# Optimization experiments

Measured on AMD Instinct MI355X. Metric: run time of the kernel, lower is better.

## Reference

```python
import jax, jax.numpy as jnp
import numpy as np

T, D, N, K, H = 2048, 4096, 32, 8, 128
ROPE_THETA = 500000.0


def setup_inputs() -> dict:
    key = jax.random.key(0)
    ks = jax.random.split(key, 5)
    s = 0.02
    return {
        "x": jax.random.normal(ks[0], (T, D), jnp.float32) * s,
        "positions": jnp.arange(T, dtype=jnp.int64 if jax.config.jax_enable_x64 else jnp.int32),
        "Wq": jax.random.normal(ks[1], (D, N, H), jnp.float32) * s,
        "Wk": jax.random.normal(ks[2], (D, K, H), jnp.float32) * s,
        "Wv": jax.random.normal(ks[3], (D, K, H), jnp.float32) * s,
        "Wo": jax.random.normal(ks[4], (N, H, D), jnp.float32) * s,
    }


def _rope(positions, q, k):
    # positions: [T]; q: [T,N,H]; k: [T,K,H]. Half-split rotation (Llama style).
    half = H // 2
    inv_freq = 1.0 / (ROPE_THETA ** (jnp.arange(0, half, dtype=jnp.float32) / half))
    ang = positions.astype(jnp.float32)[:, None] * inv_freq  # [T, H/2]
    cos = jnp.cos(ang)[:, None, :]  # [T,1,H/2]
    sin = jnp.sin(ang)[:, None, :]

    def rot(x):
        x1, x2 = x[..., :half], x[..., half:]
        return jnp.concatenate([x1 * cos - x2 * sin, x2 * cos + x1 * sin], axis=-1)

    return rot(q), rot(k)


def reference(x, positions, Wq, Wk, Wv, Wo):
    q = jnp.einsum('td,dnh->tnh', x, Wq)  # [T,N,H]
    k = jnp.einsum('td,dkh->tkh', x, Wk)  # [T,K,H]
    v = jnp.einsum('td,dkh->tkh', x, Wv)
    q, k = _rope(positions, q, k)

    rep = N // K  # GQA: expand kv heads to query heads
    kr = jnp.repeat(k, rep, axis=1)  # [T,N,H]
    vr = jnp.repeat(v, rep, axis=1)

    scale = 1.0 / jnp.sqrt(jnp.asarray(H, jnp.float32))
    scores = jnp.einsum('tnh,snh->nts', q, kr) * scale  # [N,T,T]
    causal = positions[:, None] >= positions[None, :]   # [T,T]
    scores = jnp.where(causal[None, :, :], scores, jnp.finfo(scores.dtype).min)
    probs = jax.nn.softmax(scores, axis=-1)
    ctx = jnp.einsum('nts,snh->tnh', probs, vr)  # [T,N,H]
    return jnp.einsum('tnh,nhd->td', ctx, Wo)
```

## Files before the change

kernel.cpp:

```cpp
#include <hip/hip_runtime.h>
#include <hip/hip_bf16.h>

#define T_SEQ 2048
#define D_MODEL 4096
#define N_HEADS 32
#define K_HEADS 8
#define HEAD_DIM 128

typedef unsigned short u16;
typedef short sfrag8 __attribute__((ext_vector_type(8)));
typedef float ffrag4 __attribute__((ext_vector_type(4)));

#if defined(__has_builtin)
#  if __has_builtin(__builtin_amdgcn_exp2f)
#    define EXP2F(x) __builtin_amdgcn_exp2f(x)
#  else
#    define EXP2F(x) exp2f(x)
#  endif
#else
#  define EXP2F(x) exp2f(x)
#endif

#define QSCALE_LOG2E 0.12751744900463627f
#define NEG_L2_THETA_64 (-0.29580575889569f)

__device__ __forceinline__ float bf2f(u16 u) {
    return __uint_as_float(((unsigned int)u) << 16);
}
__device__ __forceinline__ u16 f2bf(float f) {
    unsigned int x = __float_as_uint(f);
    unsigned int r = (x + 0x7fffu + ((x >> 16) & 1u)) >> 16;
    return (u16)r;
}
__device__ __forceinline__ uint4 pack8(const float4 a, const float4 b) {
    uint4 r;
    r.x = (unsigned)f2bf(a.x) | ((unsigned)f2bf(a.y) << 16);
    r.y = (unsigned)f2bf(a.z) | ((unsigned)f2bf(a.w) << 16);
    r.z = (unsigned)f2bf(b.x) | ((unsigned)f2bf(b.y) << 16);
    r.w = (unsigned)f2bf(b.z) | ((unsigned)f2bf(b.w) << 16);
    return r;
}

__device__ __forceinline__ void gload_lds16(const u16* g, u16* l) {
    __builtin_amdgcn_global_load_lds(
        (const __attribute__((address_space(1))) void*)g,
        (__attribute__((address_space(3))) void*)l, 16, 0, 0);
}

__global__ __launch_bounds__(256) void convert_bf16(
    const float* __restrict__ X, u16* __restrict__ Y, int n8)
{
    const int i = blockIdx.x * 256 + threadIdx.x;
    if (i < n8) {
        float4 a = ((const float4*)X)[(size_t)i * 2];
        float4 b = ((const float4*)X)[(size_t)i * 2 + 1];
        ((uint4*)Y)[i] = pack8(a, b);
    }
}

__global__ __launch_bounds__(256) void transpose_f32_bf16(
    const float* __restrict__ W, u16* __restrict__ WT, int R, int C)
{
    __shared__ float Ts[64][65];
    const int t = threadIdx.x;
    const int c0 = blockIdx.x * 64, r0 = blockIdx.y * 64;
    const int rl = t >> 4, cl = (t & 15) * 4;
#pragma unroll
    for (int p = 0; p < 4; ++p) {
        const int r = p * 16 + rl;
        float4 v = *(const float4*)(W + (size_t)(r0 + r) * C + c0 + cl);
        Ts[r][cl] = v.x; Ts[r][cl + 1] = v.y; Ts[r][cl + 2] = v.z; Ts[r][cl + 3] = v.w;
    }
    __syncthreads();
    const int nl = t >> 2, k4 = (t & 3) * 16;
    u16 tmp[16];
#pragma unroll
    for (int j = 0; j < 16; ++j) tmp[j] = f2bf(Ts[k4 + j][nl]);
    u16* dst = WT + (size_t)(c0 + nl) * R + r0 + k4;
    *(uint4*)(dst) = *(uint4*)&tmp[0];
    *(uint4*)(dst + 8) = *(uint4*)&tmp[8];
}

template <int CMODE>
__global__ __launch_bounds__(256) void gemm_bt(
    const u16* __restrict__ A, const u16* __restrict__ BT,
    void* __restrict__ Cp, int M, int Nb, int Kd, int ldc)
{
    __shared__ __align__(16) u16 SmemAll[2 * 128 * 64];
    u16* As = SmemAll;
    u16* Bs = SmemAll + 128 * 64;

    const int tid = threadIdx.x;
    const int lane = tid & 63;
    const int w = tid >> 6;
    const int wm = w >> 1, wn = w & 1;
    const int ln = lane & 15, quad = lane >> 4;

    int wid = blockIdx.y * gridDim.x + blockIdx.x;
    const int nwg = gridDim.x * gridDim.y;
    const int cpx = nwg >> 3;
    wid = (wid & 7) * cpx + (wid >> 3);
    const int bx = wid % gridDim.x;
    const int by = wid / gridDim.x;

    const int m0 = by * 128, n0 = bx * 128;

    size_t aoff[4], boff[4];
#pragma unroll
    for (int i = 0; i < 4; ++i) {
        const int row = (i * 4 + w) * 8 + (lane >> 3);
        const int cg = (lane & 7) ^ (lane >> 3);
        aoff[i] = (size_t)(m0 + row) * Kd + cg * 8;
        boff[i] = (size_t)(n0 + row) * Kd + cg * 8;
    }

    ffrag4 acc[4][4];
#pragma unroll
    for (int mi = 0; mi < 4; ++mi)
#pragma unroll
        for (int ni = 0; ni < 4; ++ni) acc[mi][ni] = (ffrag4){0.f, 0.f, 0.f, 0.f};

    for (int k0 = 0; k0 < Kd; k0 += 64) {
#pragma unroll
        for (int i = 0; i < 4; ++i) {
            gload_lds16(A + aoff[i] + k0, &As[(i * 4 + w) * 512]);
            gload_lds16(BT + boff[i] + k0, &Bs[(i * 4 + w) * 512]);
        }
        __syncthreads();

#pragma unroll
        for (int kk = 0; kk < 2; ++kk) {
            sfrag8 af[4], bfv[4];
#pragma unroll
            for (int mi = 0; mi < 4; ++mi) {
                const int row = wm * 64 + mi * 16 + ln;
                const int pc = ((kk * 4) | quad) ^ (ln & 7);
                af[mi] = *(const sfrag8*)&As[row * 64 + pc * 8];
            }
#pragma unroll
            for (int ni = 0; ni < 4; ++ni) {
                const int row = wn * 64 + ni * 16 + ln;
                const int pc = ((kk * 4) | quad) ^ (ln & 7);
                bfv[ni] = *(const sfrag8*)&Bs[row * 64 + pc * 8];
            }
#pragma unroll
            for (int mi = 0; mi < 4; ++mi)
#pragma unroll
                for (int ni = 0; ni < 4; ++ni)
                    acc[mi][ni] = __builtin_amdgcn_mfma_f32_16x16x32_bf16(
                        af[mi], bfv[ni], acc[mi][ni], 0, 0, 0);
        }
        __syncthreads();
    }

    if constexpr (CMODE == 4) {
        u16* base = (u16*)Cp;
        if (n0 < 5120) {
#pragma unroll
            for (int mi = 0; mi < 4; ++mi)
#pragma unroll
                for (int ni = 0; ni < 4; ++ni) {
                    const int colL = wn * 64 + ni * 16 + ln;
#pragma unroll
                    for (int i = 0; i < 4; ++i) {
                        const int rowL = wm * 64 + mi * 16 + quad * 4 + i;
                        SmemAll[rowL * 128 + colL] = f2bf(acc[mi][ni][i]);
                    }
                }
            __syncthreads();
            float invf[4];
#pragma unroll
            for (int ni = 0; ni < 4; ++ni)
                invf[ni] = EXP2F((float)(ni * 16 + ln) * NEG_L2_THETA_64);
#pragma unroll
            for (int mi = 0; mi < 4; ++mi)
#pragma unroll
                for (int ni = 0; ni < 4; ++ni) {
                    const int colL = wn * 64 + ni * 16 + ln;
                    const int fi = colL & 63;
                    const int gcol = n0 + colL;
#pragma unroll
                    for (int i = 0; i < 4; ++i) {
                        const int rowL = wm * 64 + mi * 16 + quad * 4 + i;
                        const int grow = m0 + rowL;
                        const float x1 = bf2f(SmemAll[rowL * 128 + fi]);
                        const float x2 = bf2f(SmemAll[rowL * 128 + fi + 64]);
                        const float ang = (float)grow * invf[ni];
                        const float cw = cosf(ang);
                        const float sw = sinf(ang);
                        const float o = (wn == 0) ? (x1 * cw - x2 * sw)
                                                  : (x2 * cw + x1 * sw);
                        const u16 v = f2bf(o);
                        if (gcol < 4096) {
                            base[4194304u + (size_t)grow * 4096 + gcol] = v;
                        } else {
                            base[(size_t)grow * 1024 + (gcol - 4096)] = v;
                        }
                    }
                }
        } else {
#pragma unroll
            for (int mi = 0; mi < 4; ++mi)
#pragma unroll
                for (int ni = 0; ni < 4; ++ni) {
                    const int gcol = n0 + wn * 64 + ni * 16 + ln;
#pragma unroll
                    for (int i = 0; i < 4; ++i) {
                        const int grow = m0 + wm * 64 + mi * 16 + quad * 4 + i;
                        base[2097152u + (size_t)(gcol - 5120) * T_SEQ + grow] =
                            f2bf(acc[mi][ni][i]);
                    }
                }
        }
        return;
    }

#pragma unroll
    for (int mi = 0; mi < 4; ++mi) {
#pragma unroll
        for (int ni = 0; ni < 4; ++ni) {
            const int gcol = n0 + wn * 64 + ni * 16 + ln;
#pragma unroll
            for (int i = 0; i < 4; ++i) {
                const int grow = m0 + wm * 64 + mi * 16 + quad * 4 + i;
                if constexpr (CMODE == 1) {
                    ((float*)Cp)[(size_t)grow * ldc + gcol] = acc[mi][ni][i];
                } else {
                    ((u16*)Cp)[(size_t)grow * ldc + gcol] = f2bf(acc[mi][ni][i]);
                }
            }
        }
    }
}

template <int AMODE, int CMODE>
__global__ __launch_bounds__(256) void gemm_any(
    const void* __restrict__ Ap, const float* __restrict__ B, void* __restrict__ Cp,
    int M, int Nb, int Kd, int ldc)
{
    __shared__ __align__(16) u16 As[64 * 64];
    __shared__ __align__(16) u16 Bs[64 * 72];

    const int tid = threadIdx.x;
    const int n0 = blockIdx.x * 64, m0 = blockIdx.y * 64;

    const int lr = tid >> 3;
    const int cc8 = tid & 7;
    const int sw = ((cc8 ^ (lr & 7)) * 8);
    const int dstA0 = lr * 64 + sw;
    const int dstA1 = (lr + 32) * 64 + sw;
    const size_t arow0 = (size_t)(m0 + lr) * Kd;
    const size_t arow1 = (size_t)(m0 + lr + 32) * Kd;

    const int kr = tid >> 2;
    const int ncb = (tid & 3) * 16;

    const int lane = tid & 63;
    const int w = tid >> 6;
    const int col16 = lane & 15;
    const int quad = lane >> 4;
    const int swl = lane & 7;
    const int mrow = w * 16 + col16;

    ffrag4 acc[4];
#pragma unroll
    for (int j = 0; j < 4; ++j) acc[j] = (ffrag4){0.f, 0.f, 0.f, 0.f};

    for (int k0 = 0; k0 < Kd; k0 += 64) {
        if constexpr (AMODE == 1) {
            const u16* Af = (const u16*)Ap;
            uint4 va0 = *(const uint4*)(Af + arow0 + k0 + cc8 * 8);
            uint4 va1 = *(const uint4*)(Af + arow1 + k0 + cc8 * 8);
            *(uint4*)&As[dstA0] = va0;
            *(uint4*)&As[dstA1] = va1;
        } else {
            const float* Af = (const float*)Ap;
            float4 a00 = *(const float4*)(Af + arow0 + k0 + cc8 * 8);
            float4 a01 = *(const float4*)(Af + arow0 + k0 + cc8 * 8 + 4);
            float4 a10 = *(const float4*)(Af + arow1 + k0 + cc8 * 8);
            float4 a11 = *(const float4*)(Af + arow1 + k0 + cc8 * 8 + 4);
            *(uint4*)&As[dstA0] = pack8(a00, a01);
            *(uint4*)&As[dstA1] = pack8(a10, a11);
        }
        {
            const float* bp = B + (size_t)(k0 + kr) * Nb + n0 + ncb;
            float4 b0 = *(const float4*)(bp);
            float4 b1 = *(const float4*)(bp + 4);
            float4 b2 = *(const float4*)(bp + 8);
            float4 b3 = *(const float4*)(bp + 12);
            u16 tmp[16];
            tmp[0] = f2bf(b0.x); tmp[1] = f2bf(b0.y); tmp[2] = f2bf(b0.z); tmp[3] = f2bf(b0.w);
            tmp[4] = f2bf(b1.x); tmp[5] = f2bf(b1.y); tmp[6] = f2bf(b1.z); tmp[7] = f2bf(b1.w);
            tmp[8] = f2bf(b2.x); tmp[9] = f2bf(b2.y); tmp[10] = f2bf(b2.z); tmp[11] = f2bf(b2.w);
            tmp[12] = f2bf(b3.x); tmp[13] = f2bf(b3.y); tmp[14] = f2bf(b3.z); tmp[15] = f2bf(b3.w);
#pragma unroll
            for (int e = 0; e < 16; ++e)
                Bs[(ncb + e) * 72 + kr] = tmp[e];
        }
        __syncthreads();
#pragma unroll
        for (int c = 0; c < 2; ++c) {
            const int cc = c * 4 + quad;
            const int koffA = (cc ^ swl) * 8;
            sfrag8 af = *(const sfrag8*)&As[mrow * 64 + koffA];
#pragma unroll
            for (int j = 0; j < 4; ++j) {
                sfrag8 bfv = *(const sfrag8*)&Bs[(j * 16 + col16) * 72 + cc * 8];
                acc[j] = __builtin_amdgcn_mfma_f32_16x16x32_bf16(af, bfv, acc[j], 0, 0, 0);
            }
        }
        __syncthreads();
    }

#pragma unroll
    for (int j = 0; j < 4; ++j) {
        const int gcol = n0 + j * 16 + col16;
#pragma unroll
        for (int i = 0; i < 4; ++i) {
            const int grow = m0 + w * 16 + quad * 4 + i;
            if constexpr (CMODE == 1) {
                ((float*)Cp)[(size_t)grow * ldc + gcol] = acc[j][i];
            } else if constexpr (CMODE == 2) {
                ((u16*)Cp)[(size_t)gcol * ldc + grow] = f2bf(acc[j][i]);
            } else {
                ((u16*)Cp)[(size_t)grow * ldc + gcol] = f2bf(acc[j][i]);
            }
        }
    }
}

__global__ __launch_bounds__(64) void rope_kernel(
    u16* __restrict__ buf, int nheads, int t0)
{
    const int h = blockIdx.x;
    const int t = blockIdx.y;
    u16* rowp = buf + ((size_t)t * nheads + h) * HEAD_DIM;
    const int i = threadIdx.x;
    const float p = (float)(t0 + t);
    const float inv = expf(-((float)i * (1.0f / 64.0f)) * 13.122363377404329f);
    const float ang = p * inv;
    const float c = cosf(ang);
    const float s = sinf(ang);
    const float x1 = bf2f(rowp[i]);
    const float x2 = bf2f(rowp[i + 64]);
    rowp[i] = f2bf(x1 * c - x2 * s);
    rowp[i + 64] = f2bf(x2 * c + x1 * s);
}

__global__ __launch_bounds__(256) void attn_mfma(
    const u16* q, const u16* __restrict__ k,
    const u16* __restrict__ vt, u16* ctx, int t0)
{
    __shared__ __align__(16) u16 Ktb[2][64 * 128];
    __shared__ __align__(16) u16 Vtb[2][128 * 64];
    __shared__ __align__(16) u16 Ps[4][16 * 72];

    const int head = blockIdx.x;
    const int qt = gridDim.y - 1 - blockIdx.y;
    const int kvh = head >> 2;
    const int tid = threadIdx.x;
    const int lane = tid & 63;
    const int w = tid >> 6;
    const int ln = lane & 15;
    const int quad = lane >> 4;

    const int qrow_loc = qt * 64 + w * 16 + ln;
    sfrag8 qf[4];
    {
        const u16* qg = q + ((size_t)qrow_loc * N_HEADS + head) * HEAD_DIM;
#pragma unroll
        for (int kk = 0; kk < 4; ++kk)
            qf[kk] = *(const sfrag8*)(qg + kk * 32 + quad * 8);
    }

    const int krow_l = lane >> 4;
    const int kcl    = lane & 15;
    const int vrow_l = lane >> 3;
    const int vcl    = lane & 7;

    auto stage = [&](int kv0s, int buf) {
#pragma unroll
        for (int i = 0; i < 4; ++i) {
            const int seg = i * 4 + w;
            const int krow = seg * 4 + krow_l;
            const int kcg = kcl ^ (krow & 7);
            gload_lds16(
                k + ((size_t)(kv0s + krow) * K_HEADS + kvh) * HEAD_DIM + kcg * 8,
                &Ktb[buf][seg * 512]);
            const int vrow = seg * 8 + vrow_l;
            const int vcg = vcl ^ (vrow & 7);
            gload_lds16(
                vt + ((size_t)(kvh * 128 + vrow)) * T_SEQ + kv0s + vcg * 8,
                &Vtb[buf][seg * 512]);
        }
    };

    ffrag4 acc_o[8];
#pragma unroll
    for (int dt = 0; dt < 8; ++dt) acc_o[dt] = (ffrag4){0.f, 0.f, 0.f, 0.f};
    float mrow[4] = {-INFINITY, -INFINITY, -INFINITY, -INFINITY};
    float lrow_l[4] = {0.f, 0.f, 0.f, 0.f};

    const int Tq0 = t0 + qt * 64;
    const int nst = Tq0 / 64 + 1;
    const int qabs_base = Tq0 + w * 16 + quad * 4;

    stage(0, 0);
    int cur = 0;

    for (int st = 0; st < nst; ++st) {
        const int kv0 = st * 64;
        const bool diag = (st == nst - 1);

        __syncthreads();
        if (st + 1 < nst) stage(kv0 + 64, cur ^ 1);

        const int ktc = diag ? ((w < 2) ? 2 : 4) : 4;
        ffrag4 sacc[4];
        __builtin_amdgcn_s_setprio(1);
#pragma unroll
        for (int kt = 0; kt < 4; ++kt) {
            if (kt >= ktc) break;
            sacc[kt] = (ffrag4){0.f, 0.f, 0.f, 0.f};
#pragma unroll
            for (int kk = 0; kk < 4; ++kk) {
                sfrag8 bfr = *(const sfrag8*)&Ktb[cur][
                    (kt * 16 + ln) * 128 + (((kk * 4 + quad) ^ (ln & 7)) * 8)];
                sacc[kt] = __builtin_amdgcn_mfma_f32_16x16x32_bf16(qf[kk], bfr, sacc[kt], 0, 0, 0);
            }
        }
        __builtin_amdgcn_s_setprio(0);
        float sv[4][4];
#pragma unroll
        for (int kt = 0; kt < 4; ++kt) {
            if (kt >= ktc) break;
            const int key_abs = kv0 + kt * 16 + ln;
#pragma unroll
            for (int i = 0; i < 4; ++i) {
                float s = sacc[kt][i] * QSCALE_LOG2E;
                if (diag && key_abs > qabs_base + i) s = -INFINITY;
                sv[kt][i] = s;
            }
        }
        bool grew = false;
#pragma unroll
        for (int kt = 0; kt < 4; ++kt) {
            if (kt >= ktc) break;
#pragma unroll
            for (int i = 0; i < 4; ++i)
                grew |= (sv[kt][i] > mrow[i] + 8.0f);
        }
        if (__any(grew)) {
            float tm[4];
#pragma unroll
            for (int i = 0; i < 4; ++i) {
                float t = sv[0][i];
                for (int kt = 1; kt < ktc; ++kt) t = fmaxf(t, sv[kt][i]);
                t = fmaxf(t, __shfl_xor(t, 1));
                t = fmaxf(t, __shfl_xor(t, 2));
                t = fmaxf(t, __shfl_xor(t, 4));
                t = fmaxf(t, __shfl_xor(t, 8));
                tm[i] = t;
            }
            float alpha[4];
#pragma unroll
            for (int i = 0; i < 4; ++i) {
                const float mn = fmaxf(mrow[i], tm[i]);
                alpha[i] = EXP2F(mrow[i] - mn);
                mrow[i] = mn;
            }
            const bool noop = (alpha[0] == 1.f) && (alpha[1] == 1.f) &&
                              (alpha[2] == 1.f) && (alpha[3] == 1.f);
            if (!__all(noop)) {
#pragma unroll
                for (int i = 0; i < 4; ++i) {
                    lrow_l[i] *= alpha[i];
#pragma unroll
                    for (int dt = 0; dt < 8; ++dt) acc_o[dt][i] *= alpha[i];
                }
            }
        }
#pragma unroll
        for (int kt = 0; kt < 4; ++kt) {
            if (kt >= ktc) break;
#pragma unroll
            for (int i = 0; i < 4; ++i) {
                const float p = EXP2F(sv[kt][i] - mrow[i]);
                lrow_l[i] += p;
                Ps[w][(quad * 4 + i) * 72 + kt * 16 + ln] = f2bf(p);
            }
        }
        const int kbm = ktc >> 1;
        __builtin_amdgcn_s_setprio(1);
#pragma unroll
        for (int kb = 0; kb < 2; ++kb) {
            if (kb >= kbm) break;
            sfrag8 afr = *(const sfrag8*)&Ps[w][ln * 72 + kb * 32 + quad * 8];
#pragma unroll
            for (int dt = 0; dt < 8; ++dt) {
                sfrag8 bfr = *(const sfrag8*)&Vtb[cur][
                    (dt * 16 + ln) * 64 + (((kb * 4 + quad) ^ (ln & 7)) * 8)];
                acc_o[dt] = __builtin_amdgcn_mfma_f32_16x16x32_bf16(afr, bfr, acc_o[dt], 0, 0, 0);
            }
        }
        __builtin_amdgcn_s_setprio(0);
        cur ^= 1;
    }

    float invl[4];
#pragma unroll
    for (int i = 0; i < 4; ++i) {
        float t = lrow_l[i];
        t += __shfl_xor(t, 1);
        t += __shfl_xor(t, 2);
        t += __shfl_xor(t, 4);
        t += __shfl_xor(t, 8);
        invl[i] = 1.0f / t;
    }
#pragma unroll
    for (int i = 0; i < 4; ++i) {
        u16* og = ctx + ((size_t)(qt * 64 + w * 16 + quad * 4 + i) * N_HEADS + head) * HEAD_DIM;
#pragma unroll
        for (int dt = 0; dt < 8; ++dt)
            og[dt * 16 + ln] = f2bf(acc_o[dt][i] * invl[i]);
    }
}

extern "C" void kernel_launch(void* const* d_in, const int* in_sizes, int n_in,
                              void* d_out, int out_size, void* d_ws, size_t ws_size,
                              hipStream_t stream) {
    (void)in_sizes; (void)n_in; (void)out_size;
    const float* x  = (const float*)d_in[0];
    const float* Wq = (const float*)d_in[2];
    const float* Wk = (const float*)d_in[3];
    const float* Wv = (const float*)d_in[4];
    const float* Wo = (const float*)d_in[5];
    float* out = (float*)d_out;
    char* ws = (char*)d_ws;
    const size_t MiB = 1024 * 1024;

    if (ws_size >= 88 * MiB) {
        u16* kbuf  = (u16*)(ws);
        u16* vtbuf = (u16*)(ws + 4 * MiB);
        u16* qsl   = (u16*)(ws + 8 * MiB);
        u16* xb    = (u16*)(ws + 24 * MiB);
        u16* WqkvT = (u16*)(ws + 40 * MiB);

        convert_bf16<<<dim3(T_SEQ * D_MODEL / 8 / 256), 256, 0, stream>>>(
            x, xb, T_SEQ * D_MODEL / 8);
        transpose_f32_bf16<<<dim3(64, 64), 256, 0, stream>>>(
            Wq, WqkvT, D_MODEL, N_HEADS * HEAD_DIM);
        transpose_f32_bf16<<<dim3(16, 64), 256, 0, stream>>>(
            Wk, WqkvT + (size_t)4096 * 4096, D_MODEL, K_HEADS * HEAD_DIM);
        transpose_f32_bf16<<<dim3(16, 64), 256, 0, stream>>>(
            Wv, WqkvT + (size_t)5120 * 4096, D_MODEL, K_HEADS * HEAD_DIM);

        gemm_bt<4><<<dim3(48, 16), 256, 0, stream>>>(
            xb, WqkvT, ws, T_SEQ, 6144, D_MODEL, 0);

        attn_mfma<<<dim3(N_HEADS, T_SEQ / 64), 256, 0, stream>>>(
            qsl, kbuf, vtbuf, qsl, 0);

        transpose_f32_bf16<<<dim3(64, 64), 256, 0, stream>>>(
            Wo, WqkvT, N_HEADS * HEAD_DIM, D_MODEL);
        gemm_bt<1><<<dim3(32, 16), 256, 0, stream>>>(
            qsl, WqkvT, out, T_SEQ, D_MODEL, N_HEADS * HEAD_DIM, D_MODEL);
        return;
    }

    u16* kbuf  = (u16*)(ws);
    u16* vtbuf = (u16*)(ws + 4194304);
    u16* qsl   = (u16*)(ws + 8388608);

    int S = 8;
    if (ws_size >= (size_t)8388608 + 16777216)      S = 1;
    else if (ws_size >= (size_t)8388608 + 8388608)  S = 2;
    else if (ws_size >= (size_t)8388608 + 4194304)  S = 4;
    const int Ts = T_SEQ / S;

    gemm_any<0, 0><<<dim3(16, T_SEQ / 64), 256, 0, stream>>>(
        x, Wk, kbuf, T_SEQ, K_HEADS * HEAD_DIM, D_MODEL, K_HEADS * HEAD_DIM);
    gemm_any<0, 2><<<dim3(16, T_SEQ / 64), 256, 0, stream>>>(
        x, Wv, vtbuf, T_SEQ, K_HEADS * HEAD_DIM, D_MODEL, T_SEQ);
    rope_kernel<<<dim3(K_HEADS, T_SEQ), 64, 0, stream>>>(kbuf, K_HEADS, 0);

    for (int s = 0; s < S; ++s) {
        const int t0 = s * Ts;
        gemm_any<0, 0><<<dim3(64, Ts / 64), 256, 0, stream>>>(
            x + (size_t)t0 * D_MODEL, Wq, qsl, Ts, D_MODEL, D_MODEL, D_MODEL);
        rope_kernel<<<dim3(N_HEADS, Ts), 64, 0, stream>>>(qsl, N_HEADS, t0);
        attn_mfma<<<dim3(N_HEADS, Ts / 64), 256, 0, stream>>>(
            qsl, kbuf, vtbuf, qsl, t0);
        gemm_any<1, 1><<<dim3(64, Ts / 64), 256, 0, stream>>>(
            qsl, Wo, out + (size_t)t0 * D_MODEL, Ts, D_MODEL, N_HEADS * HEAD_DIM, D_MODEL);
    }
}
```

Before: 508.9 us.

## Use 128-row query tiles in attention and fuse weight preparation kernels

```diff
diff --git a/kernel.cpp b/kernel.cpp
--- a/kernel.cpp
+++ b/kernel.cpp
@@ -77,6 +77,48 @@
 #pragma unroll
     for (int j = 0; j < 16; ++j) tmp[j] = f2bf(Ts[k4 + j][nl]);
     u16* dst = WT + (size_t)(c0 + nl) * R + r0 + k4;
+    *(uint4*)(dst) = *(uint4*)&tmp[0];
+    *(uint4*)(dst + 8) = *(uint4*)&tmp[8];
+}
+
+__global__ __launch_bounds__(256) void prep_all(
+    const float* __restrict__ x, const float* __restrict__ Wq,
+    const float* __restrict__ Wk, const float* __restrict__ Wv,
+    const float* __restrict__ Wo, u16* __restrict__ xb,
+    u16* __restrict__ WqkvT, u16* __restrict__ WoT)
+{
+    __shared__ float Ts[64][65];
+    const int t = threadIdx.x;
+    int bid = blockIdx.x;
+
+    if (bid < 4096) {
+        const int i = bid * 256 + t;
+        float4 a = ((const float4*)x)[(size_t)i * 2];
+        float4 b = ((const float4*)x)[(size_t)i * 2 + 1];
+        ((uint4*)xb)[i] = pack8(a, b);
+        return;
+    }
+    bid -= 4096;
+    const float* W; u16* WT; int C, bx, by;
+    if (bid < 4096)      { W = Wq; WT = WqkvT;                         C = 4096; bx = bid & 63;          by = bid >> 6; }
+    else if (bid < 5120) { W = Wk; WT = WqkvT + (size_t)4096 * 4096;   C = 1024; bx = (bid - 4096) & 15; by = (bid - 4096) >> 4; }
+    else if (bid < 6144) { W = Wv; WT = WqkvT + (size_t)5120 * 4096;   C = 1024; bx = (bid - 5120) & 15; by = (bid - 5120) >> 4; }
+    else                 { W = Wo; WT = WoT;                           C = 4096; bx = (bid - 6144) & 63; by = (bid - 6144) >> 6; }
+
+    const int c0 = bx * 64, r0 = by * 64;
+    const int rl = t >> 4, cl = (t & 15) * 4;
+#pragma unroll
+    for (int p = 0; p < 4; ++p) {
+        const int r = p * 16 + rl;
+        float4 v = *(const float4*)(W + (size_t)(r0 + r) * C + c0 + cl);
+        Ts[r][cl] = v.x; Ts[r][cl + 1] = v.y; Ts[r][cl + 2] = v.z; Ts[r][cl + 3] = v.w;
+    }
+    __syncthreads();
+    const int nl = t >> 2, k4 = (t & 3) * 16;
+    u16 tmp[16];
+#pragma unroll
+    for (int j = 0; j < 16; ++j) tmp[j] = f2bf(Ts[k4 + j][nl]);
+    u16* dst = WT + (size_t)(c0 + nl) * 4096 + r0 + k4;
     *(uint4*)(dst) = *(uint4*)&tmp[0];
     *(uint4*)(dst + 8) = *(uint4*)&tmp[8];
 }
@@ -347,13 +389,13 @@
     rowp[i + 64] = f2bf(x2 * c + x1 * s);
 }
 
-__global__ __launch_bounds__(256) void attn_mfma(
+__global__ __launch_bounds__(512) void attn_mfma(
     const u16* q, const u16* __restrict__ k,
     const u16* __restrict__ vt, u16* ctx, int t0)
 {
     __shared__ __align__(16) u16 Ktb[2][64 * 128];
     __shared__ __align__(16) u16 Vtb[2][128 * 64];
-    __shared__ __align__(16) u16 Ps[4][16 * 72];
+    __shared__ __align__(16) u16 Ps[8][16 * 72];
 
     const int head = blockIdx.x;
     const int qt = gridDim.y - 1 - blockIdx.y;
@@ -364,7 +406,7 @@
     const int ln = lane & 15;
     const int quad = lane >> 4;
 
-    const int qrow_loc = qt * 64 + w * 16 + ln;
+    const int qrow_loc = qt * 128 + w * 16 + ln;
     sfrag8 qf[4];
     {
         const u16* qg = q + ((size_t)qrow_loc * N_HEADS + head) * HEAD_DIM;
@@ -380,8 +422,8 @@
 
     auto stage = [&](int kv0s, int buf) {
 #pragma unroll
-        for (int i = 0; i < 4; ++i) {
-            const int seg = i * 4 + w;
+        for (int i = 0; i < 2; ++i) {
+            const int seg = i * 8 + w;
             const int krow = seg * 4 + krow_l;
             const int kcg = kcl ^ (krow & 7);
             gload_lds16(
@@ -401,109 +443,113 @@
     float mrow[4] = {-INFINITY, -INFINITY, -INFINITY, -INFINITY};
     float lrow_l[4] = {0.f, 0.f, 0.f, 0.f};
 
-    const int Tq0 = t0 + qt * 64;
-    const int nst = Tq0 / 64 + 1;
+    const int Tq0 = t0 + qt * 128;
+    const int nst = Tq0 / 64 + 2;
     const int qabs_base = Tq0 + w * 16 + quad * 4;
+    const int qlast = Tq0 + w * 16 + 15;
 
     stage(0, 0);
     int cur = 0;
 
     for (int st = 0; st < nst; ++st) {
         const int kv0 = st * 64;
-        const bool diag = (st == nst - 1);
 
         __syncthreads();
         if (st + 1 < nst) stage(kv0 + 64, cur ^ 1);
 
-        const int ktc = diag ? ((w < 2) ? 2 : 4) : 4;
-        ffrag4 sacc[4];
-        __builtin_amdgcn_s_setprio(1);
-#pragma unroll
-        for (int kt = 0; kt < 4; ++kt) {
-            if (kt >= ktc) break;
-            sacc[kt] = (ffrag4){0.f, 0.f, 0.f, 0.f};
-#pragma unroll
-            for (int kk = 0; kk < 4; ++kk) {
-                sfrag8 bfr = *(const sfrag8*)&Ktb[cur][
-                    (kt * 16 + ln) * 128 + (((kk * 4 + quad) ^ (ln & 7)) * 8)];
-                sacc[kt] = __builtin_amdgcn_mfma_f32_16x16x32_bf16(qf[kk], bfr, sacc[kt], 0, 0, 0);
-            }
-        }
-        __builtin_amdgcn_s_setprio(0);
-        float sv[4][4];
-#pragma unroll
-        for (int kt = 0; kt < 4; ++kt) {
-            if (kt >= ktc) break;
-            const int key_abs = kv0 + kt * 16 + ln;
-#pragma unroll
-            for (int i = 0; i < 4; ++i) {
-                float s = sacc[kt][i] * QSCALE_LOG2E;
-                if (diag && key_abs > qabs_base + i) s = -INFINITY;
-                sv[kt][i] = s;
-            }
-        }
-        bool grew = false;
-#pragma unroll
-        for (int kt = 0; kt < 4; ++kt) {
-            if (kt >= ktc) break;
-#pragma unroll
-            for (int i = 0; i < 4; ++i)
-                grew |= (sv[kt][i] > mrow[i] + 8.0f);
-        }
-        if (__any(grew)) {
-            float tm[4];
-#pragma unroll
-            for (int i = 0; i < 4; ++i) {
-                float t = sv[0][i];
-                for (int kt = 1; kt < ktc; ++kt) t = fmaxf(t, sv[kt][i]);
-                t = fmaxf(t, __shfl_xor(t, 1));
-                t = fmaxf(t, __shfl_xor(t, 2));
-                t = fmaxf(t, __shfl_xor(t, 4));
-                t = fmaxf(t, __shfl_xor(t, 8));
-                tm[i] = t;
-            }
-            float alpha[4];
-#pragma unroll
-            for (int i = 0; i < 4; ++i) {
-                const float mn = fmaxf(mrow[i], tm[i]);
-                alpha[i] = EXP2F(mrow[i] - mn);
-                mrow[i] = mn;
-            }
-            const bool noop = (alpha[0] == 1.f) && (alpha[1] == 1.f) &&
-                              (alpha[2] == 1.f) && (alpha[3] == 1.f);
-            if (!__all(noop)) {
+        const int d = qlast - kv0;
+        if (d >= 0) {
+            const int ktc = (d >= 32) ? 4 : 2;
+            const bool msk = (d <= 63);
+            ffrag4 sacc[4];
+            __builtin_amdgcn_s_setprio(1);
+#pragma unroll
+            for (int kt = 0; kt < 4; ++kt) {
+                if (kt >= ktc) break;
+                sacc[kt] = (ffrag4){0.f, 0.f, 0.f, 0.f};
+#pragma unroll
+                for (int kk = 0; kk < 4; ++kk) {
+                    sfrag8 bfr = *(const sfrag8*)&Ktb[cur][
+                        (kt * 16 + ln) * 128 + (((kk * 4 + quad) ^ (ln & 7)) * 8)];
+                    sacc[kt] = __builtin_amdgcn_mfma_f32_16x16x32_bf16(qf[kk], bfr, sacc[kt], 0, 0, 0);
+                }
+            }
+            __builtin_amdgcn_s_setprio(0);
+            float sv[4][4];
+#pragma unroll
+            for (int kt = 0; kt < 4; ++kt) {
+                if (kt >= ktc) break;
+                const int key_abs = kv0 + kt * 16 + ln;
 #pragma unroll
                 for (int i = 0; i < 4; ++i) {
-                    lrow_l[i] *= alpha[i];
-#pragma unroll
-                    for (int dt = 0; dt < 8; ++dt) acc_o[dt][i] *= alpha[i];
-                }
-            }
-        }
-#pragma unroll
-        for (int kt = 0; kt < 4; ++kt) {
-            if (kt >= ktc) break;
-#pragma unroll
-            for (int i = 0; i < 4; ++i) {
-                const float p = EXP2F(sv[kt][i] - mrow[i]);
-                lrow_l[i] += p;
-                Ps[w][(quad * 4 + i) * 72 + kt * 16 + ln] = f2bf(p);
-            }
-        }
-        const int kbm = ktc >> 1;
-        __builtin_amdgcn_s_setprio(1);
-#pragma unroll
-        for (int kb = 0; kb < 2; ++kb) {
-            if (kb >= kbm) break;
-            sfrag8 afr = *(const sfrag8*)&Ps[w][ln * 72 + kb * 32 + quad * 8];
-#pragma unroll
-            for (int dt = 0; dt < 8; ++dt) {
-                sfrag8 bfr = *(const sfrag8*)&Vtb[cur][
-                    (dt * 16 + ln) * 64 + (((kb * 4 + quad) ^ (ln & 7)) * 8)];
-                acc_o[dt] = __builtin_amdgcn_mfma_f32_16x16x32_bf16(afr, bfr, acc_o[dt], 0, 0, 0);
-            }
-        }
-        __builtin_amdgcn_s_setprio(0);
+                    float s = sacc[kt][i] * QSCALE_LOG2E;
+                    if (msk && key_abs > qabs_base + i) s = -INFINITY;
+                    sv[kt][i] = s;
+                }
+            }
+            bool grew = false;
+#pragma unroll
+            for (int kt = 0; kt < 4; ++kt) {
+                if (kt >= ktc) break;
+#pragma unroll
+                for (int i = 0; i < 4; ++i)
+                    grew |= (sv[kt][i] > mrow[i] + 8.0f);
+            }
+            if (__any(grew)) {
+                float tm[4];
+#pragma unroll
+                for (int i = 0; i < 4; ++i) {
+                    float t = sv[0][i];
+                    for (int kt = 1; kt < ktc; ++kt) t = fmaxf(t, sv[kt][i]);
+                    t = fmaxf(t, __shfl_xor(t, 1));
+                    t = fmaxf(t, __shfl_xor(t, 2));
+                    t = fmaxf(t, __shfl_xor(t, 4));
+                    t = fmaxf(t, __shfl_xor(t, 8));
+                    tm[i] = t;
+                }
+                float alpha[4];
+#pragma unroll
+                for (int i = 0; i < 4; ++i) {
+                    const float mn = fmaxf(mrow[i], tm[i]);
+                    alpha[i] = EXP2F(mrow[i] - mn);
+                    mrow[i] = mn;
+                }
+                const bool noop = (alpha[0] == 1.f) && (alpha[1] == 1.f) &&
+                                  (alpha[2] == 1.f) && (alpha[3] == 1.f);
+                if (!__all(noop)) {
+#pragma unroll
+                    for (int i = 0; i < 4; ++i) {
+                        lrow_l[i] *= alpha[i];
+#pragma unroll
+                        for (int dt = 0; dt < 8; ++dt) acc_o[dt][i] *= alpha[i];
+                    }
+                }
+            }
+#pragma unroll
+            for (int kt = 0; kt < 4; ++kt) {
+                if (kt >= ktc) break;
+#pragma unroll
+                for (int i = 0; i < 4; ++i) {
+                    const float p = EXP2F(sv[kt][i] - mrow[i]);
+                    lrow_l[i] += p;
+                    Ps[w][(quad * 4 + i) * 72 + kt * 16 + ln] = f2bf(p);
+                }
+            }
+            const int kbm = ktc >> 1;
+            __builtin_amdgcn_s_setprio(1);
+#pragma unroll
+            for (int kb = 0; kb < 2; ++kb) {
+                if (kb >= kbm) break;
+                sfrag8 afr = *(const sfrag8*)&Ps[w][ln * 72 + kb * 32 + quad * 8];
+#pragma unroll
+                for (int dt = 0; dt < 8; ++dt) {
+                    sfrag8 bfr = *(const sfrag8*)&Vtb[cur][
+                        (dt * 16 + ln) * 64 + (((kb * 4 + quad) ^ (ln & 7)) * 8)];
+                    acc_o[dt] = __builtin_amdgcn_mfma_f32_16x16x32_bf16(afr, bfr, acc_o[dt], 0, 0, 0);
+                }
+            }
+            __builtin_amdgcn_s_setprio(0);
+        }
         cur ^= 1;
     }
 
@@ -519,7 +565,7 @@
     }
 #pragma unroll
     for (int i = 0; i < 4; ++i) {
-        u16* og = ctx + ((size_t)(qt * 64 + w * 16 + quad * 4 + i) * N_HEADS + head) * HEAD_DIM;
+        u16* og = ctx + ((size_t)(qt * 128 + w * 16 + quad * 4 + i) * N_HEADS + head) * HEAD_DIM;
 #pragma unroll
         for (int dt = 0; dt < 8; ++dt)
             og[dt * 16 + ln] = f2bf(acc_o[dt][i] * invl[i]);
@@ -545,26 +591,24 @@
         u16* qsl   = (u16*)(ws + 8 * MiB);
         u16* xb    = (u16*)(ws + 24 * MiB);
         u16* WqkvT = (u16*)(ws + 40 * MiB);
-
-        convert_bf16<<<dim3(T_SEQ * D_MODEL / 8 / 256), 256, 0, stream>>>(
-            x, xb, T_SEQ * D_MODEL / 8);
-        transpose_f32_bf16<<<dim3(64, 64), 256, 0, stream>>>(
-            Wq, WqkvT, D_MODEL, N_HEADS * HEAD_DIM);
-        transpose_f32_bf16<<<dim3(16, 64), 256, 0, stream>>>(
-            Wk, WqkvT + (size_t)4096 * 4096, D_MODEL, K_HEADS * HEAD_DIM);
-        transpose_f32_bf16<<<dim3(16, 64), 256, 0, stream>>>(
-            Wv, WqkvT + (size_t)5120 * 4096, D_MODEL, K_HEADS * HEAD_DIM);
+        u16* WoT   = (u16*)(ws + 88 * MiB);
+        const bool doWo = (ws_size >= 120 * MiB);
+
+        prep_all<<<dim3(doWo ? 14336 : 10240), 256, 0, stream>>>(
+            x, Wq, Wk, Wv, Wo, xb, WqkvT, WoT);
 
         gemm_bt<4><<<dim3(48, 16), 256, 0, stream>>>(
             xb, WqkvT, ws, T_SEQ, 6144, D_MODEL, 0);
 
-        attn_mfma<<<dim3(N_HEADS, T_SEQ / 64), 256, 0, stream>>>(
+        attn_mfma<<<dim3(N_HEADS, T_SEQ / 128), 512, 0, stream>>>(
             qsl, kbuf, vtbuf, qsl, 0);
 
-        transpose_f32_bf16<<<dim3(64, 64), 256, 0, stream>>>(
-            Wo, WqkvT, N_HEADS * HEAD_DIM, D_MODEL);
+        if (!doWo) {
+            transpose_f32_bf16<<<dim3(64, 64), 256, 0, stream>>>(
+                Wo, WqkvT, N_HEADS * HEAD_DIM, D_MODEL);
+        }
         gemm_bt<1><<<dim3(32, 16), 256, 0, stream>>>(
-            qsl, WqkvT, out, T_SEQ, D_MODEL, N_HEADS * HEAD_DIM, D_MODEL);
+            qsl, doWo ? WoT : WqkvT, out, T_SEQ, D_MODEL, N_HEADS * HEAD_DIM, D_MODEL);
         return;
     }
 
@@ -589,7 +633,7 @@
         gemm_any<0, 0><<<dim3(64, Ts / 64), 256, 0, stream>>>(
             x + (size_t)t0 * D_MODEL, Wq, qsl, Ts, D_MODEL, D_MODEL, D_MODEL);
         rope_kernel<<<dim3(N_HEADS, Ts), 64, 0, stream>>>(qsl, N_HEADS, t0);
-        attn_mfma<<<dim3(N_HEADS, Ts / 64), 256, 0, stream>>>(
+        attn_mfma<<<dim3(N_HEADS, Ts / 128), 512, 0, stream>>>(
             qsl, kbuf, vtbuf, qsl, t0);
         gemm_any<1, 1><<<dim3(64, Ts / 64), 256, 0, stream>>>(
             qsl, Wo, out + (size_t)t0 * D_MODEL, Ts, D_MODEL, N_HEADS * HEAD_DIM, D_MODEL);
```

Measured after the change: 527.0 us. 1.04x slower.
